# Optimization experiments

Measured on AMD Instinct MI355X. Metric: run time of the kernel, lower is better.

The kernel has to match this reference:

```python
import jax, jax.numpy as jnp
import numpy as np

B, T, F = 64, 128, 9            # batch, seq_len, n_feature_fields
N_FEATURES = 32000              # vocab for embedding (N_FEATURES-1 rows) and fc head
EMB = 8
H = 16                          # lstm hidden size
IN0 = (F - 1) * EMB + 1         # lstm layer-0 input size = 65


def setup_inputs() -> dict:
    key = jax.random.key(0)
    ks = jax.random.split(key, 16)
    # x: first F-1 columns are integer-valued categorical indices, last column numeric
    cat = jax.random.randint(ks[0], (B, T, F - 1), 0, N_FEATURES - 1).astype(jnp.float32)
    num = jax.random.normal(ks[1], (B, T, 1), dtype=jnp.float32)
    x = jnp.concatenate([cat, num], axis=-1)
    h0 = jnp.zeros((2, B, H), dtype=jnp.float32)
    c0 = jnp.zeros((2, B, H), dtype=jnp.float32)
    emb = jax.random.normal(ks[2], (N_FEATURES - 1, EMB), dtype=jnp.float32)
    s0 = 1.0 / np.sqrt(IN0)
    s1 = 1.0 / np.sqrt(H)
    W_ih0 = jax.random.normal(ks[3], (4 * H, IN0), dtype=jnp.float32) * s0
    W_hh0 = jax.random.normal(ks[4], (4 * H, H), dtype=jnp.float32) * s1
    b_ih0 = jax.random.normal(ks[5], (4 * H,), dtype=jnp.float32) * 0.1
    b_hh0 = jax.random.normal(ks[6], (4 * H,), dtype=jnp.float32) * 0.1
    W_ih1 = jax.random.normal(ks[7], (4 * H, H), dtype=jnp.float32) * s1
    W_hh1 = jax.random.normal(ks[8], (4 * H, H), dtype=jnp.float32) * s1
    b_ih1 = jax.random.normal(ks[9], (4 * H,), dtype=jnp.float32) * 0.1
    b_hh1 = jax.random.normal(ks[10], (4 * H,), dtype=jnp.float32) * 0.1
    fc_w = jax.random.normal(ks[11], (N_FEATURES, H), dtype=jnp.float32) * (1.0 / np.sqrt(H))
    fc_b = jax.random.normal(ks[12], (N_FEATURES,), dtype=jnp.float32) * 0.1
    return {"x": x, "h0": h0, "c0": c0, "emb": emb,
            "W_ih0": W_ih0, "W_hh0": W_hh0, "b_ih0": b_ih0, "b_hh0": b_hh0,
            "W_ih1": W_ih1, "W_hh1": W_hh1, "b_ih1": b_ih1, "b_hh1": b_hh1,
            "fc_w": fc_w, "fc_b": fc_b}


def _lstm_layer(xs, h0, c0, Wih, Whh, bih, bhh):
    # xs: [B, T, I]; PyTorch gate order: i, f, g, o
    xp = jnp.einsum('bti,gi->btg', xs, Wih) + (bih + bhh)  # [B, T, 4H]
    xp = jnp.swapaxes(xp, 0, 1)  # [T, B, 4H]

    def step(carry, xt):
        h, c = carry
        g = xt + h @ Whh.T
        i, f, gg, o = jnp.split(g, 4, axis=-1)
        c = jax.nn.sigmoid(f) * c + jax.nn.sigmoid(i) * jnp.tanh(gg)
        h = jax.nn.sigmoid(o) * jnp.tanh(c)
        return (h, c), h

    (hT, cT), ys = jax.lax.scan(step, (h0, c0), xp)
    return jnp.swapaxes(ys, 0, 1), hT, cT


def reference(x, h0, c0, emb, W_ih0, W_hh0, b_ih0, b_hh0,
              W_ih1, W_hh1, b_ih1, b_hh1, fc_w, fc_b):
    cat = x[:, :, :-1].astype(jnp.int32)          # [B, T, F-1]
    num = x[:, :, -1:]                            # [B, T, 1]
    e = emb[cat].reshape(x.shape[0], x.shape[1], -1)  # [B, T, (F-1)*EMB]
    inp = jnp.concatenate([e, num], axis=-1)      # [B, T, IN0]
    y0, h0T, c0T = _lstm_layer(inp, h0[0], c0[0], W_ih0, W_hh0, b_ih0, b_hh0)
    y1, h1T, c1T = _lstm_layer(y0, h0[1], c0[1], W_ih1, W_hh1, b_ih1, b_hh1)
    logits = jnp.einsum('bth,vh->btv', y1, fc_w) + fc_b  # [B, T, N_FEATURES]
    hN = jnp.stack([h0T, h1T], axis=0)
    cN = jnp.stack([c0T, c1T], axis=0)
    return logits, hN, cN
```

## Files before the change

kernel.cpp:

```cpp
#include <hip/hip_runtime.h>
#include <math.h>

#define BB 64
#define TT 128
#define HH 16
#define GG 64
#define IN0_ 65
#define VV 32000
#define NROWS (BB*TT)
#define RPB 16

typedef float f32x4 __attribute__((ext_vector_type(4)));

__device__ __forceinline__ float sigf(float x) {
    return 1.0f / (1.0f + __expf(-x));
}
__device__ __forceinline__ float tanhfast(float x) {
    return 1.0f - 2.0f / (__expf(2.0f * x) + 1.0f);
}

__global__ __launch_bounds__(256) void embed_xproj0(const float* __restrict__ x,
                             const float* __restrict__ emb,
                             const float* __restrict__ Wih0, const float* __restrict__ bih0,
                             const float* __restrict__ bhh0, float* __restrict__ xp0) {
    __shared__ float wsh[GG * IN0_];
    __shared__ float insh[RPB][68];
    const int tid  = threadIdx.x;
    const int row0 = blockIdx.x * RPB;

    for (int i = tid; i < GG * IN0_; i += 256) wsh[i] = Wih0[i];

    {
        int p = tid >> 1, half = tid & 1;
        int r = p >> 3, f = p & 7;
        int idx = (int)x[(size_t)(row0 + r) * 9 + f];
        const float* er = emb + (size_t)idx * 8 + half * 4;
        float4 e = *reinterpret_cast<const float4*>(er);
        float* d = &insh[r][f * 8 + half * 4];
        d[0] = e.x; d[1] = e.y; d[2] = e.z; d[3] = e.w;
    }
    if (tid < RPB) insh[tid][64] = x[(size_t)(row0 + tid) * 9 + 8];
    __syncthreads();

    const int wave = tid >> 6, g = tid & 63;
    const float bias = bih0[g] + bhh0[g];
    float acc0 = bias, acc1 = bias, acc2 = bias, acc3 = bias;
    const float* wrow = &wsh[g * IN0_];
    const float* i0 = &insh[wave * 4 + 0][0];
    const float* i1 = &insh[wave * 4 + 1][0];
    const float* i2 = &insh[wave * 4 + 2][0];
    const float* i3 = &insh[wave * 4 + 3][0];
    #pragma unroll
    for (int k = 0; k < IN0_; ++k) {
        float wk = wrow[k];
        acc0 += i0[k] * wk;
        acc1 += i1[k] * wk;
        acc2 += i2[k] * wk;
        acc3 += i3[k] * wk;
    }
    xp0[(size_t)(row0 + wave * 4 + 0) * GG + g] = acc0;
    xp0[(size_t)(row0 + wave * 4 + 1) * GG + g] = acc1;
    xp0[(size_t)(row0 + wave * 4 + 2) * GG + g] = acc2;
    xp0[(size_t)(row0 + wave * 4 + 3) * GG + g] = acc3;
}

__global__ __launch_bounds__(64) void recurrence(const float* __restrict__ xp0,
                           const float* __restrict__ h0in, const float* __restrict__ c0in,
                           const float* __restrict__ Whh0,
                           const float* __restrict__ Wih1, const float* __restrict__ Whh1,
                           const float* __restrict__ bih1, const float* __restrict__ bhh1,
                           float* __restrict__ y1, float* __restrict__ outTail) {
    const int b = blockIdx.x;
    const int g = threadIdx.x;
    const int j = g & 15;

    float w0[HH], wi1[HH], w1[HH];
    #pragma unroll
    for (int k = 0; k < HH; ++k) {
        w0[k]  = Whh0[g * HH + k];
        wi1[k] = Wih1[g * HH + k];
        w1[k]  = Whh1[g * HH + k];
    }
    const float bias1 = bih1[g] + bhh1[g];

    float h0v = h0in[b * HH + j];
    float h1v = h0in[BB * HH + b * HH + j];
    float c0v = c0in[b * HH + j];
    float c1v = c0in[BB * HH + b * HH + j];

    const float* xprow = xp0 + (size_t)b * TT * GG + g;

    {
        float aa = xprow[0], ab = 0.0f;
        #pragma unroll
        for (int k = 0; k < 8; ++k) {
            aa += __shfl(h0v, k) * w0[k];
            ab += __shfl(h0v, k + 8) * w0[k + 8];
        }
        float acc = aa + ab;
        float iv = __shfl(acc, j), fv = __shfl(acc, j + 16);
        float gv = __shfl(acc, j + 32), ov = __shfl(acc, j + 48);
        c0v = sigf(fv) * c0v + sigf(iv) * tanhfast(gv);
        h0v = sigf(ov) * tanhfast(c0v);
    }

    for (int t = 0; t < TT - 1; ++t) {
        float xpn = xprow[(size_t)(t + 1) * GG];
        float a1a = bias1, a1b = 0.0f, a1c = 0.0f, a1d = 0.0f;
        float a0a = xpn,   a0b = 0.0f;
        #pragma unroll
        for (int k = 0; k < 8; ++k) {
            float h0k  = __shfl(h0v, k);
            float h0k8 = __shfl(h0v, k + 8);
            float h1k  = __shfl(h1v, k);
            float h1k8 = __shfl(h1v, k + 8);
            a1a += h0k  * wi1[k];
            a1b += h0k8 * wi1[k + 8];
            a1c += h1k  * w1[k];
            a1d += h1k8 * w1[k + 8];
            a0a += h0k  * w0[k];
            a0b += h0k8 * w0[k + 8];
        }
        float acc1 = (a1a + a1b) + (a1c + a1d);
        float acc0 = a0a + a0b;
        float iv1 = __shfl(acc1, j), fv1 = __shfl(acc1, j + 16);
        float gv1 = __shfl(acc1, j + 32), ov1 = __shfl(acc1, j + 48);
        float iv0 = __shfl(acc0, j), fv0 = __shfl(acc0, j + 16);
        float gv0 = __shfl(acc0, j + 32), ov0 = __shfl(acc0, j + 48);
        c1v = sigf(fv1) * c1v + sigf(iv1) * tanhfast(gv1);
        h1v = sigf(ov1) * tanhfast(c1v);
        c0v = sigf(fv0) * c0v + sigf(iv0) * tanhfast(gv0);
        h0v = sigf(ov0) * tanhfast(c0v);
        if (g < HH) y1[(size_t)(b * TT + t) * HH + g] = h1v;
    }

    {
        float a1a = bias1, a1b = 0.0f, a1c = 0.0f, a1d = 0.0f;
        #pragma unroll
        for (int k = 0; k < 8; ++k) {
            float h0k  = __shfl(h0v, k);
            float h0k8 = __shfl(h0v, k + 8);
            float h1k  = __shfl(h1v, k);
            float h1k8 = __shfl(h1v, k + 8);
            a1a += h0k  * wi1[k];
            a1b += h0k8 * wi1[k + 8];
            a1c += h1k  * w1[k];
            a1d += h1k8 * w1[k + 8];
        }
        float acc1 = (a1a + a1b) + (a1c + a1d);
        float iv1 = __shfl(acc1, j), fv1 = __shfl(acc1, j + 16);
        float gv1 = __shfl(acc1, j + 32), ov1 = __shfl(acc1, j + 48);
        c1v = sigf(fv1) * c1v + sigf(iv1) * tanhfast(gv1);
        h1v = sigf(ov1) * tanhfast(c1v);
        if (g < HH) y1[(size_t)(b * TT + TT - 1) * HH + g] = h1v;
    }

    if (g < HH) {
        outTail[b * HH + g]               = h0v;
        outTail[BB * HH + b * HH + g]     = h1v;
        outTail[2 * BB * HH + b * HH + g] = c0v;
        outTail[3 * BB * HH + b * HH + g] = c1v;
    }
}

__global__ __launch_bounds__(256) void fc_kernel(const float* __restrict__ y1,
                          const float* __restrict__ fcw, const float* __restrict__ fcb,
                          float* __restrict__ out) {
    __shared__ float ys[32 * HH];
    const int tid  = threadIdx.x;
    const int v0   = blockIdx.x * 1024 + tid * 4;
    const int row0 = blockIdx.y * 32;

    ys[tid]       = y1[row0 * HH + tid];
    ys[tid + 256] = y1[row0 * HH + 256 + tid];
    __syncthreads();

    if (v0 >= VV) return;

    float w[4][HH];
    #pragma unroll
    for (int jj = 0; jj < 4; ++jj) {
        const float4* wp = reinterpret_cast<const float4*>(fcw + (size_t)(v0 + jj) * HH);
        float4 a = wp[0], b = wp[1], c = wp[2], d = wp[3];
        w[jj][0]=a.x; w[jj][1]=a.y; w[jj][2]=a.z; w[jj][3]=a.w;
        w[jj][4]=b.x; w[jj][5]=b.y; w[jj][6]=b.z; w[jj][7]=b.w;
        w[jj][8]=c.x; w[jj][9]=c.y; w[jj][10]=c.z; w[jj][11]=c.w;
        w[jj][12]=d.x; w[jj][13]=d.y; w[jj][14]=d.z; w[jj][15]=d.w;
    }
    const float4 bias = *reinterpret_cast<const float4*>(fcb + v0);
    const f32x4* ysv = reinterpret_cast<const f32x4*>(ys);

    float* orow = out + (size_t)row0 * VV + v0;
    #pragma unroll 4
    for (int r = 0; r < 32; ++r) {
        f32x4 y0 = ysv[r * 4 + 0];
        f32x4 y1v = ysv[r * 4 + 1];
        f32x4 y2 = ysv[r * 4 + 2];
        f32x4 y3 = ysv[r * 4 + 3];
        float a0 = bias.x, a1 = bias.y, a2 = bias.z, a3 = bias.w;
        #pragma unroll
        for (int jj = 0; jj < 4; ++jj) {
            float* wj = w[jj];
            float acc = y0.x*wj[0] + y0.y*wj[1] + y0.z*wj[2] + y0.w*wj[3]
                      + y1v.x*wj[4] + y1v.y*wj[5] + y1v.z*wj[6] + y1v.w*wj[7]
                      + y2.x*wj[8] + y2.y*wj[9] + y2.z*wj[10] + y2.w*wj[11]
                      + y3.x*wj[12] + y3.y*wj[13] + y3.z*wj[14] + y3.w*wj[15];
            if (jj == 0) a0 += acc;
            else if (jj == 1) a1 += acc;
            else if (jj == 2) a2 += acc;
            else a3 += acc;
        }
        f32x4 o;
        o.x = a0; o.y = a1; o.z = a2; o.w = a3;
        __builtin_nontemporal_store(o, reinterpret_cast<f32x4*>(orow));
        orow += VV;
    }
}

extern "C" void kernel_launch(void* const* d_in, const int* in_sizes, int n_in,
                              void* d_out, int out_size, void* d_ws, size_t ws_size,
                              hipStream_t stream) {
    const float* x    = (const float*)d_in[0];
    const float* h0   = (const float*)d_in[1];
    const float* c0   = (const float*)d_in[2];
    const float* emb  = (const float*)d_in[3];
    const float* Wih0 = (const float*)d_in[4];
    const float* Whh0 = (const float*)d_in[5];
    const float* bih0 = (const float*)d_in[6];
    const float* bhh0 = (const float*)d_in[7];
    const float* Wih1 = (const float*)d_in[8];
    const float* Whh1 = (const float*)d_in[9];
    const float* bih1 = (const float*)d_in[10];
    const float* bhh1 = (const float*)d_in[11];
    const float* fcw  = (const float*)d_in[12];
    const float* fcb  = (const float*)d_in[13];

    float* out = (float*)d_out;
    float* xp0 = (float*)d_ws;
    float* y1  = xp0 + (size_t)NROWS * GG + GG;
    float* outTail = out + (size_t)NROWS * VV;

    embed_xproj0<<<NROWS / RPB, 256, 0, stream>>>(x, emb, Wih0, bih0, bhh0, xp0);
    recurrence<<<BB, 64, 0, stream>>>(xp0, h0, c0, Whh0, Wih1, Whh1, bih1, bhh1, y1, outTail);
    fc_kernel<<<dim3(32, NROWS / 32), 256, 0, stream>>>(y1, fcw, fcb, out);
}
```

Measured before the change: 290.6 us.

## Fuse embedding and layer-0 input projection into the recurrence kernel via LDS

```diff
diff --git a/kernel.cpp b/kernel.cpp
--- a/kernel.cpp
+++ b/kernel.cpp
@@ -8,7 +8,7 @@
 #define IN0_ 65
 #define VV 32000
 #define NROWS (BB*TT)
-#define RPB 16
+#define RSTRIDE 68
 
 typedef float f32x4 __attribute__((ext_vector_type(4)));
 
@@ -19,61 +19,68 @@
     return 1.0f - 2.0f / (__expf(2.0f * x) + 1.0f);
 }
 
-__global__ __launch_bounds__(256) void embed_xproj0(const float* __restrict__ x,
-                             const float* __restrict__ emb,
-                             const float* __restrict__ Wih0, const float* __restrict__ bih0,
-                             const float* __restrict__ bhh0, float* __restrict__ xp0) {
-    __shared__ float wsh[GG * IN0_];
-    __shared__ float insh[RPB][68];
-    const int tid  = threadIdx.x;
-    const int row0 = blockIdx.x * RPB;
-
-    for (int i = tid; i < GG * IN0_; i += 256) wsh[i] = Wih0[i];
-
-    {
-        int p = tid >> 1, half = tid & 1;
-        int r = p >> 3, f = p & 7;
-        int idx = (int)x[(size_t)(row0 + r) * 9 + f];
-        const float* er = emb + (size_t)idx * 8 + half * 4;
-        float4 e = *reinterpret_cast<const float4*>(er);
-        float* d = &insh[r][f * 8 + half * 4];
-        d[0] = e.x; d[1] = e.y; d[2] = e.z; d[3] = e.w;
-    }
-    if (tid < RPB) insh[tid][64] = x[(size_t)(row0 + tid) * 9 + 8];
-    __syncthreads();
-
-    const int wave = tid >> 6, g = tid & 63;
-    const float bias = bih0[g] + bhh0[g];
-    float acc0 = bias, acc1 = bias, acc2 = bias, acc3 = bias;
-    const float* wrow = &wsh[g * IN0_];
-    const float* i0 = &insh[wave * 4 + 0][0];
-    const float* i1 = &insh[wave * 4 + 1][0];
-    const float* i2 = &insh[wave * 4 + 2][0];
-    const float* i3 = &insh[wave * 4 + 3][0];
-    #pragma unroll
-    for (int k = 0; k < IN0_; ++k) {
-        float wk = wrow[k];
-        acc0 += i0[k] * wk;
-        acc1 += i1[k] * wk;
-        acc2 += i2[k] * wk;
-        acc3 += i3[k] * wk;
-    }
-    xp0[(size_t)(row0 + wave * 4 + 0) * GG + g] = acc0;
-    xp0[(size_t)(row0 + wave * 4 + 1) * GG + g] = acc1;
-    xp0[(size_t)(row0 + wave * 4 + 2) * GG + g] = acc2;
-    xp0[(size_t)(row0 + wave * 4 + 3) * GG + g] = acc3;
-}
-
-__global__ __launch_bounds__(64) void recurrence(const float* __restrict__ xp0,
+__global__ __launch_bounds__(256) void fused_front(const float* __restrict__ x,
+                           const float* __restrict__ emb,
+                           const float* __restrict__ Wih0, const float* __restrict__ bih0,
+                           const float* __restrict__ bhh0,
                            const float* __restrict__ h0in, const float* __restrict__ c0in,
                            const float* __restrict__ Whh0,
                            const float* __restrict__ Wih1, const float* __restrict__ Whh1,
                            const float* __restrict__ bih1, const float* __restrict__ bhh1,
                            float* __restrict__ y1, float* __restrict__ outTail) {
-    const int b = blockIdx.x;
-    const int g = threadIdx.x;
+    __shared__ float insh[TT * RSTRIDE];
+    __shared__ float wsh[GG * IN0_];
+    const int b   = blockIdx.x;
+    const int tid = threadIdx.x;
+    const int wave = tid >> 6, g = tid & 63;
+    const float* xb = x + (size_t)b * TT * 9;
+
+    for (int i = tid; i < GG * IN0_ / 4; i += 256) {
+        float4 wv = *reinterpret_cast<const float4*>(Wih0 + i * 4);
+        wsh[i*4+0] = wv.x; wsh[i*4+1] = wv.y; wsh[i*4+2] = wv.z; wsh[i*4+3] = wv.w;
+    }
+    #pragma unroll
+    for (int it = 0; it < 8; ++it) {
+        int q = tid + it * 256;
+        int p = q >> 1, half = q & 1;
+        int r = p >> 3, f = p & 7;
+        int idx = (int)xb[r * 9 + f];
+        const float* er = emb + (size_t)idx * 8 + half * 4;
+        float4 e = *reinterpret_cast<const float4*>(er);
+        float* d = &insh[r * RSTRIDE + f * 8 + half * 4];
+        d[0] = e.x; d[1] = e.y; d[2] = e.z; d[3] = e.w;
+    }
+    if (tid < TT) insh[tid * RSTRIDE + 64] = xb[tid * 9 + 8];
+    __syncthreads();
+
+    {
+        float wreg[IN0_];
+        #pragma unroll
+        for (int k = 0; k < IN0_; ++k) wreg[k] = wsh[g * IN0_ + k];
+        const float bias0 = bih0[g] + bhh0[g];
+        for (int r = 0; r < 32; ++r) {
+            const int row = wave * 32 + r;
+            const float* ir = &insh[row * RSTRIDE];
+            float a0 = bias0, a1 = 0.0f, a2 = 0.0f, a3 = 0.0f;
+            #pragma unroll
+            for (int k4 = 0; k4 < 16; ++k4) {
+                f32x4 v = *reinterpret_cast<const f32x4*>(ir + k4 * 4);
+                float p0 = v.x * wreg[k4*4+0] + v.y * wreg[k4*4+1]
+                         + v.z * wreg[k4*4+2] + v.w * wreg[k4*4+3];
+                if ((k4 & 3) == 0) a0 += p0;
+                else if ((k4 & 3) == 1) a1 += p0;
+                else if ((k4 & 3) == 2) a2 += p0;
+                else a3 += p0;
+            }
+            float acc = (a0 + a1) + (a2 + a3) + ir[64] * wreg[64];
+            insh[row * RSTRIDE + g] = acc;
+        }
+    }
+    __syncthreads();
+
+    if (tid >= 64) return;
+
     const int j = g & 15;
-
     float w0[HH], wi1[HH], w1[HH];
     #pragma unroll
     for (int k = 0; k < HH; ++k) {
@@ -88,10 +95,8 @@
     float c0v = c0in[b * HH + j];
     float c1v = c0in[BB * HH + b * HH + j];
 
-    const float* xprow = xp0 + (size_t)b * TT * GG + g;
-
     {
-        float aa = xprow[0], ab = 0.0f;
+        float aa = insh[g], ab = 0.0f;
         #pragma unroll
         for (int k = 0; k < 8; ++k) {
             aa += __shfl(h0v, k) * w0[k];
@@ -105,9 +110,9 @@
     }
 
     for (int t = 0; t < TT - 1; ++t) {
-        float xpn = xprow[(size_t)(t + 1) * GG];
+        float xpn = insh[(t + 1) * RSTRIDE + g];
         float a1a = bias1, a1b = 0.0f, a1c = 0.0f, a1d = 0.0f;
-        float a0a = xpn,   a0b = 0.0f;
+        float a0a = 0.0f,  a0b = 0.0f;
         #pragma unroll
         for (int k = 0; k < 8; ++k) {
             float h0k  = __shfl(h0v, k);
@@ -122,7 +127,7 @@
             a0b += h0k8 * w0[k + 8];
         }
         float acc1 = (a1a + a1b) + (a1c + a1d);
-        float acc0 = a0a + a0b;
+        float acc0 = xpn + a0a + a0b;
         float iv1 = __shfl(acc1, j), fv1 = __shfl(acc1, j + 16);
         float gv1 = __shfl(acc1, j + 32), ov1 = __shfl(acc1, j + 48);
         float iv0 = __shfl(acc0, j), fv0 = __shfl(acc0, j + 16);
@@ -212,7 +217,7 @@
         }
         f32x4 o;
         o.x = a0; o.y = a1; o.z = a2; o.w = a3;
-        __builtin_nontemporal_store(o, reinterpret_cast<f32x4*>(orow));
+        *reinterpret_cast<f32x4*>(orow) = o;
         orow += VV;
     }
 }
@@ -236,11 +241,10 @@
     const float* fcb  = (const float*)d_in[13];
 
     float* out = (float*)d_out;
-    float* xp0 = (float*)d_ws;
-    float* y1  = xp0 + (size_t)NROWS * GG + GG;
+    float* y1  = (float*)d_ws;
     float* outTail = out + (size_t)NROWS * VV;
 
-    embed_xproj0<<<NROWS / RPB, 256, 0, stream>>>(x, emb, Wih0, bih0, bhh0, xp0);
-    recurrence<<<BB, 64, 0, stream>>>(xp0, h0, c0, Whh0, Wih1, Whh1, bih1, bhh1, y1, outTail);
+    fused_front<<<BB, 256, 0, stream>>>(x, emb, Wih0, bih0, bhh0, h0, c0,
+                                        Whh0, Wih1, Whh1, bih1, bhh1, y1, outTail);
     fc_kernel<<<dim3(32, NROWS / 32), 256, 0, stream>>>(y1, fcw, fcb, out);
 }
```

After: 303.7 us. +4.5%, slower.
